# Kernel tuning notes

Measured on AMD Instinct MI355X. Metric: run time of the kernel, lower is better.

## Reference

```python
import jax, jax.numpy as jnp
import numpy as np

# Hyperparameters (match init_kwargs)
P = 168          # window
M1, M2, M3 = 2, 3, 4
HIDC = 32        # hidCNN
CK = 6           # CNN_kernel
HIDR = 100       # hidRNN
HIDS = 5         # hidSkip
SKIP = 24
HW = 24          # highway_window
B = 128
L = P - CK + 1                 # 163, band-summed sequence length
PT = int((P - CK) / SKIP)      # int(6.75) = 6, matches torch int(self.pt)
M = M1 * M2 * M3


def setup_inputs() -> dict:
    key = jax.random.key(0)
    ks = jax.random.split(key, 16)
    def rn(k, shape, scale):
        return jax.random.normal(k, shape, dtype=jnp.float32) * scale
    return {
        "x": jax.random.normal(ks[0], (B, P, M1, M2, M3), dtype=jnp.float32),
        # Conv3d(P, P*HIDC*CK, kernel=(m1,m2,m3)) weight/bias
        "conv_w": rn(ks[1], (P * HIDC * CK, P, M1, M2, M3), 0.02),
        "conv_b": rn(ks[2], (P * HIDC * CK,), 0.02),
        # GRU1: input HIDC, hidden HIDR (torch layout: [3H, I], [3H, H])
        "gru1_Wih": rn(ks[3], (3 * HIDR, HIDC), 0.05),
        "gru1_Whh": rn(ks[4], (3 * HIDR, HIDR), 0.05),
        "gru1_bih": rn(ks[5], (3 * HIDR,), 0.05),
        "gru1_bhh": rn(ks[6], (3 * HIDR,), 0.05),
        # GRUskip: input HIDC, hidden HIDS
        "grus_Wih": rn(ks[7], (3 * HIDS, HIDC), 0.05),
        "grus_Whh": rn(ks[8], (3 * HIDS, HIDS), 0.05),
        "grus_bih": rn(ks[9], (3 * HIDS,), 0.05),
        "grus_bhh": rn(ks[10], (3 * HIDS,), 0.05),
        # linear1: (HIDR + SKIP*HIDS) -> M
        "lin1_w": rn(ks[11], (M, HIDR + SKIP * HIDS), 0.05),
        "lin1_b": rn(ks[12], (M,), 0.05),
        # highway: HW -> 1
        "hw_w": rn(ks[13], (1, HW), 0.05),
        "hw_b": rn(ks[14], (1,), 0.05),
    }


def _gru_last(x_seq, Wih, Whh, bih, bhh, hid):
    """PyTorch-equation GRU over [T, B, I]; returns final hidden [B, hid]."""
    h0 = jnp.zeros((x_seq.shape[1], hid), x_seq.dtype)
    def step(h, xt):
        gi = xt @ Wih.T + bih            # [B, 3H]
        gh = h @ Whh.T + bhh             # [B, 3H]
        ir, iz, inn = jnp.split(gi, 3, axis=-1)
        hr, hz, hn = jnp.split(gh, 3, axis=-1)
        r = jax.nn.sigmoid(ir + hr)
        z = jax.nn.sigmoid(iz + hz)
        n = jnp.tanh(inn + r * hn)
        h_new = (1.0 - z) * n + z * h
        return h_new, None
    h, _ = jax.lax.scan(step, h0, x_seq)
    return h


def reference(x, conv_w, conv_b,
              gru1_Wih, gru1_Whh, gru1_bih, gru1_bhh,
              grus_Wih, grus_Whh, grus_bih, grus_bhh,
              lin1_w, lin1_b, hw_w, hw_b):
    Bn = x.shape[0]
    # Conv3d with full-size spatial kernel == GEMM over (P, m1, m2, m3)
    c = jnp.einsum('bpijk,opijk->bo', x, conv_w) + conv_b    # [B, P*HIDC*CK]
    c = jax.nn.relu(c).reshape(Bn, HIDC, CK, P)
    # Diagonal-band sum: res[b,ch,t] = sum_k c[b,ch,k,k+t], t in [0, L)
    k_idx = jnp.arange(CK)[:, None]                           # [CK, 1]
    pos = k_idx + jnp.arange(L)[None, :]                      # [CK, L]
    c = c[:, :, k_idx, pos].sum(axis=2)                       # [B, HIDC, L]
    # (dropout is identity in eval mode)
    # Main GRU over time
    r = _gru_last(jnp.transpose(c, (2, 0, 1)),
                  gru1_Wih, gru1_Whh, gru1_bih, gru1_bhh, HIDR)  # [B, HIDR]
    # Skip GRU over periodic phase
    s = c[:, :, L - PT * SKIP:]                               # [B, HIDC, PT*SKIP]
    s = s.reshape(Bn, HIDC, PT, SKIP)
    s = jnp.transpose(s, (2, 0, 3, 1)).reshape(PT, Bn * SKIP, HIDC)
    hs = _gru_last(s, grus_Wih, grus_Whh, grus_bih, grus_bhh, HIDS)
    hs = hs.reshape(Bn, SKIP * HIDS)
    r = jnp.concatenate([r, hs], axis=1)                      # [B, HIDR+SKIP*HIDS]
    res = r @ lin1_w.T + lin1_b                               # [B, M]
    z = jnp.transpose(x[:, -HW:], (0, 2, 3, 4, 1)).reshape(-1, HW)  # [B*M, HW]
    z = (z @ hw_w.T + hw_b).reshape(Bn, M)
    res = jax.nn.sigmoid(res + z)                             # output_fun='sigmoid'
    return res.reshape(Bn, M1, M2, M3)
```

## Files before the change

### kernel.cpp

```cpp
#include <hip/hip_runtime.h>
#include <hip/hip_bf16.h>
#include <cstdint>

#define B_      128
#define K_      4032
#define NOUT_   32256
#define NCHUNK_ 126
#define CSTRIDE 4128768ull

typedef __attribute__((ext_vector_type(8))) short short8;
typedef __attribute__((ext_vector_type(4))) float floatx4;

__device__ __forceinline__ unsigned short f2bf(float f) {
  unsigned int u = __float_as_uint(f);
  return (unsigned short)((u + 0x7FFFu + ((u >> 16) & 1u)) >> 16);
}
__device__ __forceinline__ short8 cvt8(float4 f0, float4 f1) {
  short8 r;
  r[0] = (short)f2bf(f0.x); r[1] = (short)f2bf(f0.y);
  r[2] = (short)f2bf(f0.z); r[3] = (short)f2bf(f0.w);
  r[4] = (short)f2bf(f1.x); r[5] = (short)f2bf(f1.y);
  r[6] = (short)f2bf(f1.z); r[7] = (short)f2bf(f1.w);
  return r;
}
__device__ __forceinline__ float sigm(float x) { return 1.f / (1.f + __expf(-x)); }

__device__ __forceinline__ void gl_lds16(const void* g, void* l) {
  __builtin_amdgcn_global_load_lds(
      (const __attribute__((address_space(1))) void*)g,
      (__attribute__((address_space(3))) void*)l, 16, 0, 0);
}

__global__ void prep_k(const float* __restrict__ x, unsigned short* __restrict__ Apack) {
  int idx = blockIdx.x * 256 + threadIdx.x;
  int b = idx / K_;
  int k = idx - b * K_;
  unsigned short v = f2bf(x[idx]);
  int kc = k >> 5, qq = (k >> 3) & 3, j = k & 7, mt = b >> 4, r = b & 15;
  Apack[(size_t)(((kc * 8 + mt) * 64) + qq * 16 + r) * 8 + j] = v;
}

__global__ __launch_bounds__(256, 3) void gemm_k(const unsigned short* __restrict__ Ap,
    const float* __restrict__ W, float* __restrict__ Cpart, int kchunks) {
  __shared__ unsigned short Albs[2][4096];
  __shared__ float4 Wlds[2][1024];

  const int tid  = threadIdx.x;
  const int lane = tid & 63;
  const int w    = tid >> 6;
  const int q    = lane >> 4;
  const int l7   = lane & 7;

  const int slice = blockIdx.x / 252;
  const int n0    = (blockIdx.x - slice * 252) * 128;
  const int kbase = slice * kchunks;

  floatx4 zero = {0.f, 0.f, 0.f, 0.f};
  floatx4 acc[8][2];
#pragma unroll
  for (int mt = 0; mt < 8; mt++) { acc[mt][0] = zero; acc[mt][1] = zero; }

  auto stage = [&](int buf, int kc_glob) {
#pragma unroll
    for (int i = 0; i < 2; i++) {
      int j = w * 2 + i;
      const char* g = (const char*)Ap + (size_t)kc_glob * 8192 + j * 1024 + lane * 16;
      gl_lds16(g, (char*)Albs[buf] + j * 1024);
    }
#pragma unroll
    for (int i = 0; i < 4; i++) {
      int j = w * 4 + i;
      int nloc = j * 8 + (lane >> 3);
      int quad = (lane & 7) ^ ((lane >> 3) & 7);
      const float* g = W + (size_t)(n0 + nloc) * K_ + kc_glob * 32 + quad * 4;
      gl_lds16(g, &Wlds[buf][j * 64]);
    }
  };

  stage(0, kbase);
  __syncthreads();

  for (int kc = 0; kc < kchunks; kc++) {
    int pb = kc & 1;
    if (kc + 1 < kchunks) stage(pb ^ 1, kbase + kc + 1);

    short8 a[8];
    const short8* Ab = (const short8*)Albs[pb];
#pragma unroll
    for (int mt = 0; mt < 8; mt++) a[mt] = Ab[mt * 64 + lane];

    short8 bf[2];
    const float4* Wb = Wlds[pb];
#pragma unroll
    for (int nt = 0; nt < 2; nt++) {
      int n = w * 32 + nt * 16 + (lane & 15);
      float4 lo = Wb[n * 8 + ((2 * q) ^ l7)];
      float4 hi = Wb[n * 8 + ((2 * q + 1) ^ l7)];
      bf[nt] = cvt8(lo, hi);
    }
#pragma unroll
    for (int mt = 0; mt < 8; mt++) {
#pragma unroll
      for (int nt = 0; nt < 2; nt++)
        acc[mt][nt] = __builtin_amdgcn_mfma_f32_16x16x32_bf16(a[mt], bf[nt], acc[mt][nt], 0, 0, 0);
    }
    __syncthreads();
  }

  float* Cp = Cpart + (size_t)slice * CSTRIDE;
#pragma unroll
  for (int mt = 0; mt < 8; mt++) {
#pragma unroll
    for (int nt = 0; nt < 2; nt++) {
      int n = n0 + w * 32 + nt * 16 + (lane & 15);
#pragma unroll
      for (int r = 0; r < 4; r++) {
        int brow = mt * 16 + q * 4 + r;
        Cp[(size_t)brow * NOUT_ + n] = acc[mt][nt][r];
      }
    }
  }
}

__global__ void diag_k(const float* __restrict__ Cp, const float* __restrict__ bias,
                       float* __restrict__ c2, int nparts) {
  int idx = blockIdx.x * 256 + threadIdx.x;
  int l = idx % 163;
  int t = idx / 163;
  int h = t % 32;
  int b = t / 32;
  size_t base = (size_t)b * NOUT_ + h * 1008 + l;
  int obase = h * 1008 + l;
  float s = 0.f;
#pragma unroll
  for (int k = 0; k < 6; k++) {
    float v = bias[obase + k * 169];
    for (int p = 0; p < nparts; p++) v += Cp[(size_t)p * CSTRIDE + base + k * 169];
    s += fmaxf(v, 0.f);
  }
  c2[idx] = s;
}

__global__ __launch_bounds__(320) void recur_k(const float* __restrict__ c2,
    const float* __restrict__ W1ih, const float* __restrict__ W1hh,
    const float* __restrict__ b1ih, const float* __restrict__ b1hh,
    const float* __restrict__ Wsih, const float* __restrict__ Wshh,
    const float* __restrict__ bsih, const float* __restrict__ bshh,
    float* __restrict__ r_out, float* __restrict__ hs_out) {
  int tid = threadIdx.x;
  if (blockIdx.x < 128) {
    __shared__ float xl[163 * 32];
    __shared__ float hsh[100], rsh[100], zsh[100];
    int b = blockIdx.x;
    for (int i = tid; i < 5216; i += 320) {
      int c = i / 163, t = i - c * 163;
      xl[t * 32 + c] = c2[b * 5216 + i];
    }
    if (tid < 100) hsh[tid] = 0.f;
    float4 wi4[8], wh4[25];
    float bi = 0.f, bh = 0.f;
    if (tid < 300) {
      bi = b1ih[tid]; bh = b1hh[tid];
      const float4* p = (const float4*)(W1ih + tid * 32);
#pragma unroll
      for (int i = 0; i < 8; i++) wi4[i] = p[i];
      const float4* p2 = (const float4*)(W1hh + tid * 100);
#pragma unroll
      for (int i = 0; i < 25; i++) wh4[i] = p2[i];
    }
    __syncthreads();
    for (int t = 0; t < 163; t++) {
      float gi = 0.f, gh = 0.f;
      if (tid < 300) {
        const float4* xt = (const float4*)(xl + t * 32);
        float4 A0 = {0, 0, 0, 0}, A1 = {0, 0, 0, 0};
#pragma unroll
        for (int i = 0; i < 4; i++) A0 += wi4[i] * xt[i];
#pragma unroll
        for (int i = 4; i < 8; i++) A1 += wi4[i] * xt[i];
        float4 Ai = A0 + A1;
        gi = bi + Ai.x + Ai.y + Ai.z + Ai.w;
        const float4* h4 = (const float4*)hsh;
        float4 H0 = {0, 0, 0, 0}, H1 = {0, 0, 0, 0};
#pragma unroll
        for (int i = 0; i < 12; i++) H0 += wh4[i] * h4[i];
#pragma unroll
        for (int i = 12; i < 25; i++) H1 += wh4[i] * h4[i];
        float4 Hh = H0 + H1;
        gh = bh + Hh.x + Hh.y + Hh.z + Hh.w;
        if (tid < 100) rsh[tid] = sigm(gi + gh);
        else if (tid < 200) zsh[tid - 100] = sigm(gi + gh);
      }
      __syncthreads();
      if (tid >= 200 && tid < 300) {
        int i = tid - 200;
        float nn = tanhf(gi + rsh[i] * gh);
        float z = zsh[i];
        hsh[i] = (1.f - z) * nn + z * hsh[i];
      }
      __syncthreads();
    }
    if (tid < 100) r_out[b * 100 + tid] = hsh[tid];
  } else {
    __shared__ float wi[480], wh[75], bi2[15], bh2[15];
    for (int i = tid; i < 480; i += 320) wi[i] = Wsih[i];
    if (tid < 75) wh[tid] = Wshh[tid];
    if (tid < 15) { bi2[tid] = bsih[tid]; bh2[tid] = bshh[tid]; }
    __syncthreads();
    int row = (blockIdx.x - 128) * 320 + tid;
    if (row < 3072) {
      int b = row / 24, sk = row - b * 24;
      float h[5] = {0.f, 0.f, 0.f, 0.f, 0.f};
      for (int t = 0; t < 6; t++) {
        int l = 19 + t * 24 + sk;
        float xv[32];
#pragma unroll
        for (int c = 0; c < 32; c++) xv[c] = c2[(size_t)(b * 32 + c) * 163 + l];
        float gi[15], gh[15];
#pragma unroll
        for (int g = 0; g < 15; g++) {
          float s = bi2[g];
#pragma unroll
          for (int c = 0; c < 32; c++) s += wi[g * 32 + c] * xv[c];
          gi[g] = s;
          float s2 = bh2[g];
#pragma unroll
          for (int c = 0; c < 5; c++) s2 += wh[g * 5 + c] * h[c];
          gh[g] = s2;
        }
#pragma unroll
        for (int i = 0; i < 5; i++) {
          float r = sigm(gi[i] + gh[i]);
          float z = sigm(gi[5 + i] + gh[5 + i]);
          float nn = tanhf(gi[10 + i] + r * gh[10 + i]);
          h[i] = (1.f - z) * nn + z * h[i];
        }
      }
#pragma unroll
      for (int i = 0; i < 5; i++) hs_out[b * 120 + sk * 5 + i] = h[i];
    }
  }
}

__global__ void final_k(const float* __restrict__ x, const float* __restrict__ r_in,
    const float* __restrict__ hs, const float* __restrict__ lw,
    const float* __restrict__ lb, const float* __restrict__ hww,
    const float* __restrict__ hwb, float* __restrict__ out) {
  int idx = blockIdx.x * 256 + threadIdx.x;
  int b = idx / 24, m = idx - (idx / 24) * 24;
  float acc = lb[m] + hwb[0];
  const float* wrow = lw + m * 220;
#pragma unroll 4
  for (int i = 0; i < 100; i++) acc += r_in[b * 100 + i] * wrow[i];
#pragma unroll 4
  for (int i = 0; i < 120; i++) acc += hs[b * 120 + i] * wrow[100 + i];
#pragma unroll
  for (int t = 0; t < 24; t++) acc += x[(size_t)b * K_ + (144 + t) * 24 + m] * hww[t];
  out[idx] = sigm(acc);
}

extern "C" void kernel_launch(void* const* d_in, const int* in_sizes, int n_in,
                              void* d_out, int out_size, void* d_ws, size_t ws_size,
                              hipStream_t stream) {
  const float* x      = (const float*)d_in[0];
  const float* conv_w = (const float*)d_in[1];
  const float* conv_b = (const float*)d_in[2];
  const float* g1Wih  = (const float*)d_in[3];
  const float* g1Whh  = (const float*)d_in[4];
  const float* g1bih  = (const float*)d_in[5];
  const float* g1bhh  = (const float*)d_in[6];
  const float* gsWih  = (const float*)d_in[7];
  const float* gsWhh  = (const float*)d_in[8];
  const float* gsbih  = (const float*)d_in[9];
  const float* gsbhh  = (const float*)d_in[10];
  const float* lw     = (const float*)d_in[11];
  const float* lb     = (const float*)d_in[12];
  const float* hww    = (const float*)d_in[13];
  const float* hwb    = (const float*)d_in[14];
  float* out = (float*)d_out;

  const int nslice = (ws_size >= 53377024ull) ? 3 : 1;
  const int kchunks = NCHUNK_ / nslice;

  char* ws = (char*)d_ws;
  unsigned short* Apack = (unsigned short*)ws;
  size_t off = 1048576;
  float* Cpart = (float*)(ws + off); off += (size_t)nslice * 16515072ull;
  float* c2    = (float*)(ws + off); off += 2670592;
  float* r_out = (float*)(ws + off); off += 51200;
  float* hs    = (float*)(ws + off);

  prep_k <<<2016, 256, 0, stream>>>(x, Apack);
  gemm_k <<<252 * nslice, 256, 0, stream>>>(Apack, conv_w, Cpart, kchunks);
  diag_k <<<2608, 256, 0, stream>>>(Cpart, conv_b, c2, nslice);
  recur_k<<<138,  320, 0, stream>>>(c2, g1Wih, g1Whh, g1bih, g1bhh,
                                    gsWih, gsWhh, gsbih, gsbhh, r_out, hs);
  final_k<<<12,   256, 0, stream>>>(x, r_out, hs, lw, lb, hww, hwb, out);
}
```

Baseline: 1.014 ms.

## Precompute GRU input gates via MFMA, split-k-row recurrence, retile conv GEMM

Hoists the GRU input projection out of the sequential loop into a separate bf16 MFMA kernel (gi_k), fed by a packed-activation output from diag_k and packed weights from bpack_k. The recurrence kernel now splits each hidden unit's dot product across two threads, keeps Whh in registers, double-buffers the hidden state so there is one barrier per step instead of two, and uses a fast exp-based tanh. The conv GEMM is retiled to 64-wide N blocks with A read directly from global instead of LDS, and the slice count is fixed at 3 so it no longer depends on workspace size. The changes add extra launches and workspace, lower the input projection to bf16, and risk register spills from the large per-thread weight arrays.

```diff
diff --git a/kernel.cpp b/kernel.cpp
--- a/kernel.cpp
+++ b/kernel.cpp
@@ -5,8 +5,11 @@
 #define B_      128
 #define K_      4032
 #define NOUT_   32256
-#define NCHUNK_ 126
 #define CSTRIDE 4128768ull
+#define NSLICE  3
+#define KCH     42
+#define GIROWS  20864
+#define NTILES_GI 19
 
 typedef __attribute__((ext_vector_type(8))) short short8;
 typedef __attribute__((ext_vector_type(4))) float floatx4;
@@ -24,7 +27,11 @@
   return r;
 }
 __device__ __forceinline__ float sigm(float x) { return 1.f / (1.f + __expf(-x)); }
-
+__device__ __forceinline__ float tanh_f(float x) {
+  x = fminf(fmaxf(x, -15.f), 15.f);
+  float e = __expf(2.f * x);
+  return (e - 1.f) / (e + 1.f);
+}
 __device__ __forceinline__ void gl_lds16(const void* g, void* l) {
   __builtin_amdgcn_global_load_lds(
       (const __attribute__((address_space(1))) void*)g,
@@ -40,39 +47,44 @@
   Apack[(size_t)(((kc * 8 + mt) * 64) + qq * 16 + r) * 8 + j] = v;
 }
 
-__global__ __launch_bounds__(256, 3) void gemm_k(const unsigned short* __restrict__ Ap,
-    const float* __restrict__ W, float* __restrict__ Cpart, int kchunks) {
-  __shared__ unsigned short Albs[2][4096];
-  __shared__ float4 Wlds[2][1024];
+__global__ void bpack_k(const float* __restrict__ Wih, unsigned short* __restrict__ Bp) {
+  int t = blockIdx.x * 256 + threadIdx.x;
+  if (t >= NTILES_GI * 64 * 8) return;
+  int j = t & 7, slot = t >> 3;
+  int lane = slot & 63, nt = slot >> 6;
+  int n = nt * 16 + (lane & 15);
+  int k = (lane >> 4) * 8 + j;
+  Bp[t] = (n < 300) ? f2bf(Wih[n * 32 + k]) : (unsigned short)0;
+}
+
+__global__ __launch_bounds__(256, 5) void gemm_k(const unsigned short* __restrict__ Ap,
+    const float* __restrict__ W, float* __restrict__ Cpart) {
+  __shared__ float4 Wlds[2][512];
 
   const int tid  = threadIdx.x;
   const int lane = tid & 63;
   const int w    = tid >> 6;
   const int q    = lane >> 4;
-  const int l7   = lane & 7;
-
-  const int slice = blockIdx.x / 252;
-  const int n0    = (blockIdx.x - slice * 252) * 128;
-  const int kbase = slice * kchunks;
+
+  const int slice = blockIdx.x / 504;
+  const int nb    = blockIdx.x - slice * 504;
+  const int n0    = nb * 64;
+  const int kbase = slice * KCH;
 
   floatx4 zero = {0.f, 0.f, 0.f, 0.f};
-  floatx4 acc[8][2];
-#pragma unroll
-  for (int mt = 0; mt < 8; mt++) { acc[mt][0] = zero; acc[mt][1] = zero; }
-
-  auto stage = [&](int buf, int kc_glob) {
+  floatx4 acc[8];
+#pragma unroll
+  for (int i = 0; i < 8; i++) acc[i] = zero;
+
+  const int nloc_lo = lane >> 3;
+  const int quad_st = (lane & 7) ^ ((lane >> 3) & 7);
+
+  auto stage = [&](int buf, int kcg) {
 #pragma unroll
     for (int i = 0; i < 2; i++) {
       int j = w * 2 + i;
-      const char* g = (const char*)Ap + (size_t)kc_glob * 8192 + j * 1024 + lane * 16;
-      gl_lds16(g, (char*)Albs[buf] + j * 1024);
-    }
-#pragma unroll
-    for (int i = 0; i < 4; i++) {
-      int j = w * 4 + i;
-      int nloc = j * 8 + (lane >> 3);
-      int quad = (lane & 7) ^ ((lane >> 3) & 7);
-      const float* g = W + (size_t)(n0 + nloc) * K_ + kc_glob * 32 + quad * 4;
+      int nloc = j * 8 + nloc_lo;
+      const float* g = W + (size_t)(n0 + nloc) * K_ + kcg * 32 + quad_st * 4;
       gl_lds16(g, &Wlds[buf][j * 64]);
     }
   };
@@ -80,50 +92,42 @@
   stage(0, kbase);
   __syncthreads();
 
-  for (int kc = 0; kc < kchunks; kc++) {
+  const int nl  = w * 16 + (lane & 15);
+  const int sw0 = nl * 8 + ((2 * q)     ^ (nl & 7));
+  const int sw1 = nl * 8 + ((2 * q + 1) ^ (nl & 7));
+
+  for (int kc = 0; kc < KCH; kc++) {
     int pb = kc & 1;
-    if (kc + 1 < kchunks) stage(pb ^ 1, kbase + kc + 1);
-
+    if (kc + 1 < KCH) stage(pb ^ 1, kbase + kc + 1);
+
+    const short8* Ag = (const short8*)Ap + (size_t)(kbase + kc) * 512 + lane;
     short8 a[8];
-    const short8* Ab = (const short8*)Albs[pb];
-#pragma unroll
-    for (int mt = 0; mt < 8; mt++) a[mt] = Ab[mt * 64 + lane];
-
-    short8 bf[2];
-    const float4* Wb = Wlds[pb];
-#pragma unroll
-    for (int nt = 0; nt < 2; nt++) {
-      int n = w * 32 + nt * 16 + (lane & 15);
-      float4 lo = Wb[n * 8 + ((2 * q) ^ l7)];
-      float4 hi = Wb[n * 8 + ((2 * q + 1) ^ l7)];
-      bf[nt] = cvt8(lo, hi);
-    }
-#pragma unroll
-    for (int mt = 0; mt < 8; mt++) {
-#pragma unroll
-      for (int nt = 0; nt < 2; nt++)
-        acc[mt][nt] = __builtin_amdgcn_mfma_f32_16x16x32_bf16(a[mt], bf[nt], acc[mt][nt], 0, 0, 0);
-    }
+#pragma unroll
+    for (int mt = 0; mt < 8; mt++) a[mt] = Ag[mt * 64];
+
+    float4 lo = Wlds[pb][sw0];
+    float4 hi = Wlds[pb][sw1];
+    short8 bfr = cvt8(lo, hi);
+#pragma unroll
+    for (int mt = 0; mt < 8; mt++)
+      acc[mt] = __builtin_amdgcn_mfma_f32_16x16x32_bf16(a[mt], bfr, acc[mt], 0, 0, 0);
     __syncthreads();
   }
 
   float* Cp = Cpart + (size_t)slice * CSTRIDE;
+  const int n = n0 + nl;
 #pragma unroll
   for (int mt = 0; mt < 8; mt++) {
 #pragma unroll
-    for (int nt = 0; nt < 2; nt++) {
-      int n = n0 + w * 32 + nt * 16 + (lane & 15);
-#pragma unroll
-      for (int r = 0; r < 4; r++) {
-        int brow = mt * 16 + q * 4 + r;
-        Cp[(size_t)brow * NOUT_ + n] = acc[mt][nt][r];
-      }
+    for (int r = 0; r < 4; r++) {
+      int brow = mt * 16 + q * 4 + r;
+      Cp[(size_t)brow * NOUT_ + n] = acc[mt][r];
     }
   }
 }
 
 __global__ void diag_k(const float* __restrict__ Cp, const float* __restrict__ bias,
-                       float* __restrict__ c2, int nparts) {
+                       float* __restrict__ c2, unsigned short* __restrict__ Xp) {
   int idx = blockIdx.x * 256 + threadIdx.x;
   int l = idx % 163;
   int t = idx / 163;
@@ -135,79 +139,104 @@
 #pragma unroll
   for (int k = 0; k < 6; k++) {
     float v = bias[obase + k * 169];
-    for (int p = 0; p < nparts; p++) v += Cp[(size_t)p * CSTRIDE + base + k * 169];
+#pragma unroll
+    for (int p = 0; p < NSLICE; p++) v += Cp[(size_t)p * CSTRIDE + base + k * 169];
     s += fmaxf(v, 0.f);
   }
   c2[idx] = s;
-}
-
-__global__ __launch_bounds__(320) void recur_k(const float* __restrict__ c2,
-    const float* __restrict__ W1ih, const float* __restrict__ W1hh,
-    const float* __restrict__ b1ih, const float* __restrict__ b1hh,
+  int row = b * 163 + l;
+  int mt = row >> 4, r = row & 15, qq = h >> 3, j = h & 7;
+  Xp[(size_t)((mt * 64) + qq * 16 + r) * 8 + j] = f2bf(s);
+}
+
+__global__ void gi_k(const unsigned short* __restrict__ Xp, const unsigned short* __restrict__ Bp,
+                     const float* __restrict__ bih, const float* __restrict__ bhh,
+                     float* __restrict__ gi) {
+  int wid  = blockIdx.x * 4 + (threadIdx.x >> 6);
+  int lane = threadIdx.x & 63;
+  int mt = wid / NTILES_GI, nt = wid - mt * NTILES_GI;
+  short8 a   = *(const short8*)(Xp + (size_t)(mt * 64 + lane) * 8);
+  short8 bfr = *(const short8*)(Bp + (size_t)(nt * 64 + lane) * 8);
+  floatx4 acc = {0.f, 0.f, 0.f, 0.f};
+  acc = __builtin_amdgcn_mfma_f32_16x16x32_bf16(a, bfr, acc, 0, 0, 0);
+  int n = nt * 16 + (lane & 15), q = lane >> 4;
+  if (n < 300) {
+    float bv = bih[n] + (n < 200 ? bhh[n] : 0.f);
+#pragma unroll
+    for (int r = 0; r < 4; r++) {
+      int row = mt * 16 + q * 4 + r;
+      gi[(size_t)row * 300 + n] = acc[r] + bv;
+    }
+  }
+}
+
+__global__ __launch_bounds__(256, 1) void recur_k(const float* __restrict__ gi,
+    const float* __restrict__ Whh, const float* __restrict__ bhh,
+    const float* __restrict__ c2,
     const float* __restrict__ Wsih, const float* __restrict__ Wshh,
     const float* __restrict__ bsih, const float* __restrict__ bshh,
     float* __restrict__ r_out, float* __restrict__ hs_out) {
   int tid = threadIdx.x;
   if (blockIdx.x < 128) {
-    __shared__ float xl[163 * 32];
-    __shared__ float hsh[100], rsh[100], zsh[100];
+    __shared__ float hbuf[2][104];
     int b = blockIdx.x;
-    for (int i = tid; i < 5216; i += 320) {
-      int c = i / 163, t = i - c * 163;
-      xl[t * 32 + c] = c2[b * 5216 + i];
-    }
-    if (tid < 100) hsh[tid] = 0.f;
-    float4 wi4[8], wh4[25];
-    float bi = 0.f, bh = 0.f;
-    if (tid < 300) {
-      bi = b1ih[tid]; bh = b1hh[tid];
-      const float4* p = (const float4*)(W1ih + tid * 32);
-#pragma unroll
-      for (int i = 0; i < 8; i++) wi4[i] = p[i];
-      const float4* p2 = (const float4*)(W1hh + tid * 100);
-#pragma unroll
-      for (int i = 0; i < 25; i++) wh4[i] = p2[i];
-    }
+    bool active = tid < 200;
+    int u = tid >> 1, half = tid & 1;
+
+    float wreg[3][52];
+    if (active) {
+#pragma unroll
+      for (int g = 0; g < 3; g++) {
+        int grow = (g * 100 + u) * 100;
+#pragma unroll
+        for (int j = 0; j < 52; j++) {
+          int col = half * 48 + j;
+          float v = 0.f;
+          if (half == 0 || j >= 4) v = Whh[grow + col];
+          wreg[g][j] = v;
+        }
+      }
+    }
+    float bnh = (active && half == 0) ? bhh[200 + u] : 0.f;
+    if (tid < 104) { hbuf[0][tid] = 0.f; }
+    float hprev = 0.f;
     __syncthreads();
+
+    const float* gib = gi + (size_t)b * 163 * 300;
     for (int t = 0; t < 163; t++) {
-      float gi = 0.f, gh = 0.f;
-      if (tid < 300) {
-        const float4* xt = (const float4*)(xl + t * 32);
-        float4 A0 = {0, 0, 0, 0}, A1 = {0, 0, 0, 0};
-#pragma unroll
-        for (int i = 0; i < 4; i++) A0 += wi4[i] * xt[i];
-#pragma unroll
-        for (int i = 4; i < 8; i++) A1 += wi4[i] * xt[i];
-        float4 Ai = A0 + A1;
-        gi = bi + Ai.x + Ai.y + Ai.z + Ai.w;
-        const float4* h4 = (const float4*)hsh;
-        float4 H0 = {0, 0, 0, 0}, H1 = {0, 0, 0, 0};
-#pragma unroll
-        for (int i = 0; i < 12; i++) H0 += wh4[i] * h4[i];
-#pragma unroll
-        for (int i = 12; i < 25; i++) H1 += wh4[i] * h4[i];
-        float4 Hh = H0 + H1;
-        gh = bh + Hh.x + Hh.y + Hh.z + Hh.w;
-        if (tid < 100) rsh[tid] = sigm(gi + gh);
-        else if (tid < 200) zsh[tid - 100] = sigm(gi + gh);
+      int cur = t & 1, nxt = cur ^ 1;
+      if (active) {
+        float g0 = gib[t * 300 + u];
+        float g1 = gib[t * 300 + 100 + u];
+        float g2 = gib[t * 300 + 200 + u];
+        const float4* hp = (const float4*)&hbuf[cur][half * 48];
+        float s0 = 0.f, s1 = 0.f, s2 = bnh;
+#pragma unroll
+        for (int i = 0; i < 13; i++) {
+          float4 hv = hp[i];
+          s0 += wreg[0][4*i+0]*hv.x + wreg[0][4*i+1]*hv.y + wreg[0][4*i+2]*hv.z + wreg[0][4*i+3]*hv.w;
+          s1 += wreg[1][4*i+0]*hv.x + wreg[1][4*i+1]*hv.y + wreg[1][4*i+2]*hv.z + wreg[1][4*i+3]*hv.w;
+          s2 += wreg[2][4*i+0]*hv.x + wreg[2][4*i+1]*hv.y + wreg[2][4*i+2]*hv.z + wreg[2][4*i+3]*hv.w;
+        }
+        s0 += __shfl_xor(s0, 1);
+        s1 += __shfl_xor(s1, 1);
+        s2 += __shfl_xor(s2, 1);
+        float r = sigm(g0 + s0);
+        float z = sigm(g1 + s1);
+        float n = tanh_f(g2 + r * s2);
+        hprev = (1.f - z) * n + z * hprev;
+        hbuf[nxt][u] = hprev;
       }
       __syncthreads();
-      if (tid >= 200 && tid < 300) {
-        int i = tid - 200;
-        float nn = tanhf(gi + rsh[i] * gh);
-        float z = zsh[i];
-        hsh[i] = (1.f - z) * nn + z * hsh[i];
-      }
-      __syncthreads();
-    }
-    if (tid < 100) r_out[b * 100 + tid] = hsh[tid];
+    }
+    if (active && half == 0) r_out[b * 100 + u] = hprev;
   } else {
     __shared__ float wi[480], wh[75], bi2[15], bh2[15];
-    for (int i = tid; i < 480; i += 320) wi[i] = Wsih[i];
+    for (int i = tid; i < 480; i += 256) wi[i] = Wsih[i];
     if (tid < 75) wh[tid] = Wshh[tid];
     if (tid < 15) { bi2[tid] = bsih[tid]; bh2[tid] = bshh[tid]; }
     __syncthreads();
-    int row = (blockIdx.x - 128) * 320 + tid;
+    int row = (blockIdx.x - 128) * 256 + tid;
     if (row < 3072) {
       int b = row / 24, sk = row - b * 24;
       float h[5] = {0.f, 0.f, 0.f, 0.f, 0.f};
@@ -216,13 +245,13 @@
         float xv[32];
 #pragma unroll
         for (int c = 0; c < 32; c++) xv[c] = c2[(size_t)(b * 32 + c) * 163 + l];
-        float gi[15], gh[15];
+        float gv[15], gh[15];
 #pragma unroll
         for (int g = 0; g < 15; g++) {
           float s = bi2[g];
 #pragma unroll
           for (int c = 0; c < 32; c++) s += wi[g * 32 + c] * xv[c];
-          gi[g] = s;
+          gv[g] = s;
           float s2 = bh2[g];
 #pragma unroll
           for (int c = 0; c < 5; c++) s2 += wh[g * 5 + c] * h[c];
@@ -230,9 +259,9 @@
         }
 #pragma unroll
         for (int i = 0; i < 5; i++) {
-          float r = sigm(gi[i] + gh[i]);
-          float z = sigm(gi[5 + i] + gh[5 + i]);
-          float nn = tanhf(gi[10 + i] + r * gh[10 + i]);
+          float r = sigm(gv[i] + gh[i]);
+          float z = sigm(gv[5 + i] + gh[5 + i]);
+          float nn = tanh_f(gv[10 + i] + r * gh[10 + i]);
           h[i] = (1.f - z) * nn + z * h[i];
         }
       }
@@ -279,21 +308,24 @@
   const float* hwb    = (const float*)d_in[14];
   float* out = (float*)d_out;
 
-  const int nslice = (ws_size >= 53377024ull) ? 3 : 1;
-  const int kchunks = NCHUNK_ / nslice;
-
   char* ws = (char*)d_ws;
-  unsigned short* Apack = (unsigned short*)ws;
-  size_t off = 1048576;
-  float* Cpart = (float*)(ws + off); off += (size_t)nslice * 16515072ull;
-  float* c2    = (float*)(ws + off); off += 2670592;
-  float* r_out = (float*)(ws + off); off += 51200;
-  float* hs    = (float*)(ws + off);
-
+  size_t off = 0;
+  auto alloc = [&](size_t bytes) { size_t cur = off; off = (off + bytes + 255) & ~255ull; return cur; };
+  unsigned short* Apack = (unsigned short*)(ws + alloc(1032192));
+  float* Cpart = (float*)(ws + alloc((size_t)NSLICE * CSTRIDE * 4));
+  float* c2    = (float*)(ws + alloc(2670592));
+  unsigned short* Xp = (unsigned short*)(ws + alloc(1335296));
+  unsigned short* Bp = (unsigned short*)(ws + alloc(19456));
+  float* gi    = (float*)(ws + alloc((size_t)GIROWS * 300 * 4));
+  float* r_out = (float*)(ws + alloc(51200));
+  float* hs    = (float*)(ws + alloc(15360));
+
+  bpack_k<<<38,   256, 0, stream>>>(g1Wih, Bp);
   prep_k <<<2016, 256, 0, stream>>>(x, Apack);
-  gemm_k <<<252 * nslice, 256, 0, stream>>>(Apack, conv_w, Cpart, kchunks);
-  diag_k <<<2608, 256, 0, stream>>>(Cpart, conv_b, c2, nslice);
-  recur_k<<<138,  320, 0, stream>>>(c2, g1Wih, g1Whh, g1bih, g1bhh,
+  gemm_k <<<1512, 256, 0, stream>>>(Apack, conv_w, Cpart);
+  diag_k <<<2608, 256, 0, stream>>>(Cpart, conv_b, c2, Xp);
+  gi_k   <<<6194, 256, 0, stream>>>(Xp, Bp, g1bih, g1bhh, gi);
+  recur_k<<<140,  256, 0, stream>>>(gi, g1Whh, g1bhh, c2,
                                     gsWih, gsWhh, gsbih, gsbhh, r_out, hs);
   final_k<<<12,   256, 0, stream>>>(x, r_out, hs, lw, lb, hww, hwb, out);
 }
```

New measurement: 910.0 us. 1.11x faster.
